# Kernel optimization log

Hardware: AMD Instinct MI355X
Metric: run time of the kernel (lower is better)

The kernel has to match this reference:

```python
import jax, jax.numpy as jnp
import numpy as np

D_MODEL = 1024
N_HEADS = 16
HEAD_DIM = D_MODEL // N_HEADS


def setup_inputs() -> dict:
    key = jax.random.key(0)
    ks = jax.random.split(key, 5)
    B, T = 4, 2048
    x = jax.random.normal(ks[0], (B, T, D_MODEL), dtype=jnp.float32)
    s = 1.0 / np.sqrt(D_MODEL)
    W_qkv = jax.random.normal(ks[1], (D_MODEL, 3 * D_MODEL), dtype=jnp.float32) * s
    b_qkv = jnp.zeros((3 * D_MODEL,), dtype=jnp.float32)
    W_out = jax.random.normal(ks[2], (D_MODEL, D_MODEL), dtype=jnp.float32) * s
    b_out = jnp.zeros((D_MODEL,), dtype=jnp.float32)
    return {"x": x, "W_qkv": W_qkv, "b_qkv": b_qkv, "W_out": W_out, "b_out": b_out}


def reference(x, W_qkv, b_qkv, W_out, b_out):
    B, T, C = x.shape
    qkv = x @ W_qkv + b_qkv                      # [B,T,3C]
    q, k, v = jnp.split(qkv, 3, axis=-1)
    # [B,T,H,Dh] -> [B,H,T,Dh]
    q = q.reshape(B, T, N_HEADS, HEAD_DIM).transpose(0, 2, 1, 3)
    k = k.reshape(B, T, N_HEADS, HEAD_DIM).transpose(0, 2, 1, 3)
    v = v.reshape(B, T, N_HEADS, HEAD_DIM).transpose(0, 2, 1, 3)
    scale = HEAD_DIM ** -0.5
    attn = jnp.einsum('bhqd,bhkd->bhqk', q, k) * scale
    causal = jnp.triu(jnp.ones((T, T), dtype=bool), k=1)
    attn = jnp.where(causal, -jnp.inf, attn)
    attn = jax.nn.softmax(attn, axis=-1)
    out = jnp.einsum('bhqk,bhkd->bhqd', attn, v)
    out = out.transpose(0, 2, 1, 3).reshape(B, T, C)
    return out @ W_out + b_out
```

## Files before the change

### kernel.cpp

```cpp
#include <hip/hip_runtime.h>
#include <hip/hip_bf16.h>


typedef unsigned short u16;
typedef unsigned int u32;
typedef __attribute__((ext_vector_type(8))) short short8;
typedef __attribute__((ext_vector_type(4))) short short4v;
typedef __attribute__((ext_vector_type(4))) float f32x4;

#define N_HEADS 16
#define HEAD_DIM 64
#define TSEQ 2048
#define BATCH 4
#define MROWS (BATCH * TSEQ)
#define N3 3072

__device__ __forceinline__ void cp16(const u16* g, u16* l) {
  __builtin_amdgcn_global_load_lds((const __attribute__((address_space(1))) void*)g,
                                   (__attribute__((address_space(3))) void*)l, 16, 0, 0);
}

__device__ __forceinline__ f32x4 mfma16(short8 a, short8 b, f32x4 c) {
  return __builtin_amdgcn_mfma_f32_16x16x32_bf16(a, b, c, 0, 0, 0);
}

__device__ __forceinline__ u16 f2b(float f) {
  __hip_bfloat16 h = __float2bfloat16(f);
  return *reinterpret_cast<u16*>(&h);
}

#define PREP_CVT_BLOCKS 8192
#define PREP_WQKV_BLOCKS (96 * 32)
#define PREP_WOUT_BLOCKS (32 * 32)
#define PREP_TOTAL (PREP_CVT_BLOCKS + PREP_WQKV_BLOCKS + PREP_WOUT_BLOCKS)

__device__ __forceinline__ void transpose_tile(const float* __restrict__ src,
                                               u16* __restrict__ dst,
                                               int R, int Cn, int c0, int r0,
                                               float (*tile)[33]) {
  const int tx = threadIdx.x & 31, ty = threadIdx.x >> 5;
  for (int i = ty; i < 32; i += 8)
    tile[i][tx] = src[(size_t)(r0 + i) * Cn + c0 + tx];
  __syncthreads();
  for (int i = ty; i < 32; i += 8)
    dst[(size_t)(c0 + i) * R + r0 + tx] = f2b(tile[tx][i]);
}

__global__ __launch_bounds__(256) void prep_kernel(
    const float* __restrict__ x, u16* __restrict__ xb,
    const float* __restrict__ Wqkv, u16* __restrict__ wqkv_t,
    const float* __restrict__ Wout, u16* __restrict__ wout_t) {
  __shared__ float tile[32][33];
  const int bx = blockIdx.x;
  if (bx < PREP_CVT_BLOCKS) {
    int i = bx * 256 + threadIdx.x;
    float4 v = *(const float4*)(x + (size_t)i * 4);
    u16* d = xb + (size_t)i * 4;
    d[0] = f2b(v.x); d[1] = f2b(v.y); d[2] = f2b(v.z); d[3] = f2b(v.w);
  } else if (bx < PREP_CVT_BLOCKS + PREP_WQKV_BLOCKS) {
    int b2 = bx - PREP_CVT_BLOCKS;
    int c0 = (b2 % 96) * 32, r0 = (b2 / 96) * 32;
    transpose_tile(Wqkv, wqkv_t, 1024, N3, c0, r0, tile);
  } else {
    int b3 = bx - PREP_CVT_BLOCKS - PREP_WQKV_BLOCKS;
    int c0 = (b3 % 32) * 32, r0 = (b3 / 32) * 32;
    transpose_tile(Wout, wout_t, 1024, 1024, c0, r0, tile);
  }
}

__device__ __forceinline__ void gemm128_sync(const u16* __restrict__ A,
                                             const u16* __restrict__ Bt,
                                             int m0, int n0,
                                             u16* Asm, u16* Bsm,
                                             f32x4 acc[4][4]) {
  const int tid = threadIdx.x;
  const int w = tid >> 6;
  const int lane = tid & 63;
  const int quad = lane >> 4;
  const int l16 = lane & 15;
  const int wm = (w >> 1) * 64;
  const int wn = (w & 1) * 64;

#pragma unroll
  for (int i = 0; i < 4; ++i)
#pragma unroll
    for (int j = 0; j < 4; ++j) acc[i][j] = (f32x4){0.f, 0.f, 0.f, 0.f};

  for (int k0 = 0; k0 < 1024; k0 += 32) {
    __syncthreads();
#pragma unroll
    for (int p = 0; p < 2; ++p) {
      int s = p * 256 + tid;
      int row = s >> 2;
      int c4 = (s & 3) ^ ((row >> 1) & 3);
      cp16(A + (size_t)(m0 + row) * 1024 + k0 + c4 * 8,
           Asm + (size_t)(p * 256 + w * 64) * 8);
      cp16(Bt + (size_t)(n0 + row) * 1024 + k0 + c4 * 8,
           Bsm + (size_t)(p * 256 + w * 64) * 8);
    }
    __syncthreads();

    short8 a[4], b[4];
#pragma unroll
    for (int i = 0; i < 4; ++i) {
      int row = wm + i * 16 + l16;
      int c4 = quad ^ ((row >> 1) & 3);
      a[i] = *(const short8*)(Asm + row * 32 + c4 * 8);
    }
#pragma unroll
    for (int j = 0; j < 4; ++j) {
      int row = wn + j * 16 + l16;
      int c4 = quad ^ ((row >> 1) & 3);
      b[j] = *(const short8*)(Bsm + row * 32 + c4 * 8);
    }
#pragma unroll
    for (int i = 0; i < 4; ++i)
#pragma unroll
      for (int j = 0; j < 4; ++j)
        acc[i][j] = mfma16(a[i], b[j], acc[i][j]);
  }
}

__device__ __forceinline__ void gemm128_pipe(const u16* __restrict__ A,
                                             const u16* __restrict__ Bt,
                                             int m0, int n0,
                                             u16* Asm, u16* Bsm,
                                             f32x4 acc[4][4]) {
  const int tid = threadIdx.x;
  const int w = tid >> 6;
  const int lane = tid & 63;
  const int quad = lane >> 4;
  const int l16 = lane & 15;
  const int wm = (w >> 1) * 64;
  const int wn = (w & 1) * 64;

#pragma unroll
  for (int i = 0; i < 4; ++i)
#pragma unroll
    for (int j = 0; j < 4; ++j) acc[i][j] = (f32x4){0.f, 0.f, 0.f, 0.f};

#define STG128(k0_, b_)                                                     \
  do {                                                                      \
    _Pragma("unroll")                                                       \
    for (int p = 0; p < 2; ++p) {                                           \
      int s = p * 256 + tid;                                                \
      int row = s >> 2;                                                     \
      int c4 = (s & 3) ^ ((row >> 1) & 3);                                  \
      cp16(A + (size_t)(m0 + row) * 1024 + (k0_) + c4 * 8,                  \
           Asm + (size_t)(b_) * 4096 + (p * 256 + w * 64) * 8);             \
      cp16(Bt + (size_t)(n0 + row) * 1024 + (k0_) + c4 * 8,                 \
           Bsm + (size_t)(b_) * 4096 + (p * 256 + w * 64) * 8);             \
    }                                                                       \
  } while (0)

  STG128(0, 0);
  STG128(32, 1);
  asm volatile("s_waitcnt vmcnt(4)" ::: "memory");
  asm volatile("s_barrier" ::: "memory");

  for (int kt = 0; kt < 32; ++kt) {
    const u16* Ab = Asm + (kt & 1) * 4096;
    const u16* Bb = Bsm + (kt & 1) * 4096;
    short8 a[4], b[4];
#pragma unroll
    for (int i = 0; i < 4; ++i) {
      int row = wm + i * 16 + l16;
      int c4 = quad ^ ((row >> 1) & 3);
      a[i] = *(const short8*)(Ab + row * 32 + c4 * 8);
    }
#pragma unroll
    for (int j = 0; j < 4; ++j) {
      int row = wn + j * 16 + l16;
      int c4 = quad ^ ((row >> 1) & 3);
      b[j] = *(const short8*)(Bb + row * 32 + c4 * 8);
    }
#pragma unroll
    for (int i = 0; i < 4; ++i)
#pragma unroll
      for (int j = 0; j < 4; ++j)
        acc[i][j] = mfma16(a[i], b[j], acc[i][j]);

    asm volatile("s_barrier" ::: "memory");
    if (kt + 2 < 32) {
      STG128((kt + 2) * 32, kt & 1);
      asm volatile("s_waitcnt vmcnt(4)" ::: "memory");
    } else if (kt + 1 < 32) {
      asm volatile("s_waitcnt vmcnt(0)" ::: "memory");
    }
    asm volatile("s_barrier" ::: "memory");
  }
#undef STG128
}

__global__ __launch_bounds__(256) void gemm_qkv_kernel(
    const u16* __restrict__ x, const u16* __restrict__ Wt,
    const float* __restrict__ bias,
    u16* __restrict__ qb, u16* __restrict__ kb, u16* __restrict__ vtb) {
  __shared__ __align__(16) u16 Asm[128 * 32];
  __shared__ __align__(16) u16 Bsm[128 * 32];
  f32x4 acc[4][4];
  const int m0 = blockIdx.y * 128;
  const int n0 = blockIdx.x * 128;
  gemm128_sync(x, Wt, m0, n0, Asm, Bsm, acc);

  const int tid = threadIdx.x;
  const int w = tid >> 6, lane = tid & 63, quad = lane >> 4, l16 = lane & 15;
  const int wm = (w >> 1) * 64, wn = (w & 1) * 64;
#pragma unroll
  for (int j = 0; j < 4; ++j) {
    int col = n0 + wn + j * 16 + l16;
    float bv = bias[col];
    int which = col >> 10;
    int rem = col & 1023;
    int h = rem >> 6, d = rem & 63;
#pragma unroll
    for (int i = 0; i < 4; ++i) {
      int m4 = m0 + wm + i * 16 + quad * 4;
      int b_ = m4 >> 11, t4 = m4 & 2047;
      int bh = b_ * N_HEADS + h;
      if (which == 2) {
        short4v pk;
#pragma unroll
        for (int r = 0; r < 4; ++r) pk[r] = (short)f2b(acc[i][j][r] + bv);
        *(short4v*)(vtb + ((size_t)((bh << 6) + d)) * TSEQ + t4) = pk;
      } else {
        u16* dst = (which == 0) ? qb : kb;
#pragma unroll
        for (int r = 0; r < 4; ++r)
          dst[((size_t)(bh * TSEQ + t4 + r) << 6) + d] = f2b(acc[i][j][r] + bv);
      }
    }
  }
}

__global__ __launch_bounds__(512, 4) void attn_kernel(const u16* __restrict__ qb,
                                                      const u16* __restrict__ kb,
                                                      const u16* __restrict__ vtb,
                                                      u16* __restrict__ ob) {
  const int flat = blockIdx.y * 8 + blockIdx.x;
  const int swz = (flat & 7) * 64 + (flat >> 3);
  const int bh = swz >> 3;
  const int p  = swz & 7;
  const int qtH = 15 - p, qtL = p;
  __shared__ __align__(16) u16 Ksm[2][4096];
  __shared__ __align__(16) u16 Vsm[2][4096];
  const int tid = threadIdx.x;
  const int w = tid >> 6, lane = tid & 63, quad = lane >> 4, l16 = lane & 15;
  const int qminH = qtH * 128 + w * 16;
  const int qminL = qtL * 128 + w * 16;

  short8 qfH0, qfH1, qfL0, qfL1;
  {
    const u16* qrH = qb + ((size_t)(bh * TSEQ + qminH + l16)) * 64;
    qfH0 = *(const short8*)(qrH + quad * 8);
    qfH1 = *(const short8*)(qrH + 32 + quad * 8);
    const u16* qrL = qb + ((size_t)(bh * TSEQ + qminL + l16)) * 64;
    qfL0 = *(const short8*)(qrL + quad * 8);
    qfL1 = *(const short8*)(qrL + 32 + quad * 8);
  }

  f32x4 oH[4], oL[4];
  float lpH = 0.f, lpL = 0.f;
#pragma unroll
  for (int j = 0; j < 4; ++j) {
    oH[j] = (f32x4){0.f, 0.f, 0.f, 0.f};
    oL[j] = (f32x4){0.f, 0.f, 0.f, 0.f};
  }
  const float cexp = 0.18033688011112042f;
  const float M = 10.0f;

  const u16* kb_bh = kb + (size_t)bh * TSEQ * 64;
  const u16* vt_bh = vtb + (size_t)bh * 64 * TSEQ;
  const int nk = 2 * qtH + 2;

#define STAGE(kt_, b_)                                                        \
  do {                                                                        \
    const u16* kbase_ = kb_bh + (size_t)((kt_) * 64) * 64;                    \
    const u16* vbase_ = vt_bh + (kt_) * 64;                                   \
    int row_ = tid >> 3;                                                      \
    int c8_ = (tid & 7) ^ (row_ & 7);                                         \
    int krow_ = (row_ & 0x23) | ((row_ & 0x0C) << 1) | ((row_ & 0x10) >> 2);  \
    cp16(kbase_ + krow_ * 64 + c8_ * 8, &Ksm[b_][w * 512]);                   \
    cp16(vbase_ + (size_t)row_ * TSEQ + c8_ * 8, &Vsm[b_][w * 512]);          \
  } while (0)

#define FRAG(qmin_, qf0_, qf1_, o_, lp_)                                      \
  do {                                                                        \
    const int qlane = (qmin_) + l16;                                          \
    f32x4 s[4];                                                               \
    _Pragma("unroll")                                                         \
    for (int j = 0; j < 4; ++j) {                                             \
      int row = j * 16 + l16;                                                 \
      int ca = quad ^ (row & 7);                                              \
      int cb = (4 + quad) ^ (row & 7);                                        \
      short8 k0 = *(const short8*)(Kb + row * 64 + ca * 8);                   \
      short8 k1 = *(const short8*)(Kb + row * 64 + cb * 8);                   \
      f32x4 z = (f32x4){0.f, 0.f, 0.f, 0.f};                                  \
      z = mfma16(k0, (qf0_), z);                                              \
      z = mfma16(k1, (qf1_), z);                                              \
      s[j] = z;                                                               \
    }                                                                         \
    if (kt * 64 + 63 > (qmin_)) {                                             \
      _Pragma("unroll")                                                       \
      for (int j = 0; j < 4; ++j) {                                           \
        _Pragma("unroll")                                                     \
        for (int r = 0; r < 4; ++r) {                                         \
          int kabs = kt * 64 + ((j >> 1) << 5) + (quad << 3) + ((j & 1) << 2) + r; \
          if (kabs > qlane) s[j][r] = -1e30f;                                 \
        }                                                                     \
      }                                                                       \
    }                                                                         \
    short8 ap0, ap1;                                                          \
    _Pragma("unroll")                                                         \
    for (int j = 0; j < 4; ++j) {                                             \
      _Pragma("unroll")                                                       \
      for (int r = 0; r < 4; ++r) {                                           \
        float p_ = __builtin_amdgcn_exp2f(__builtin_fmaf(s[j][r], cexp, -M)); \
        (lp_) += p_;                                                          \
        u16 pb = f2b(p_);                                                     \
        if (j < 2) ap0[j * 4 + r] = (short)pb;                                \
        else       ap1[(j - 2) * 4 + r] = (short)pb;                          \
      }                                                                       \
    }                                                                         \
    _Pragma("unroll")                                                         \
    for (int j = 0; j < 4; ++j) {                                             \
      int row = j * 16 + l16;                                                 \
      int ca = quad ^ (row & 7);                                              \
      int cb = (4 + quad) ^ (row & 7);                                        \
      short8 v0 = *(const short8*)(Vb + row * 64 + ca * 8);                   \
      short8 v1 = *(const short8*)(Vb + row * 64 + cb * 8);                   \
      (o_)[j] = mfma16(ap0, v0, (o_)[j]);                                     \
      (o_)[j] = mfma16(ap1, v1, (o_)[j]);                                     \
    }                                                                         \
  } while (0)

  STAGE(0, 0);

  for (int kt = 0; kt < nk; ++kt) {
    asm volatile("s_barrier" ::: "memory");
    if (kt + 1 < nk) {
      STAGE(kt + 1, (kt + 1) & 1);
      asm volatile("s_waitcnt vmcnt(2)" ::: "memory");
    } else {
      asm volatile("s_waitcnt vmcnt(0)" ::: "memory");
    }
    asm volatile("s_barrier" ::: "memory");

    const u16* Kb = Ksm[kt & 1];
    const u16* Vb = Vsm[kt & 1];

    __builtin_amdgcn_s_setprio(1);
    if (kt * 64 <= qminH + 15) FRAG(qminH, qfH0, qfH1, oH, lpH);
    if (kt * 64 <= qminL + 15) FRAG(qminL, qfL0, qfL1, oL, lpL);
    __builtin_amdgcn_s_setprio(0);
  }
#undef FRAG
#undef STAGE

  const int b_ = bh >> 4, h = bh & 15;
#define EPI(qmin_, o_, lp_)                                                   \
  do {                                                                        \
    float lp = (lp_);                                                         \
    lp += __shfl_xor(lp, 16);                                                 \
    lp += __shfl_xor(lp, 32);                                                 \
    float dn[4];                                                              \
    _Pragma("unroll")                                                         \
    for (int r = 0; r < 4; ++r)                                               \
      dn[r] = __shfl(lp, (lane & 48) + quad * 4 + r);                         \
    _Pragma("unroll")                                                         \
    for (int j = 0; j < 4; ++j) {                                             \
      _Pragma("unroll")                                                       \
      for (int r = 0; r < 4; ++r) {                                           \
        int t = (qmin_) + quad * 4 + r;                                       \
        int d = j * 16 + l16;                                                 \
        ob[((size_t)(b_ * TSEQ + t)) * 1024 + h * 64 + d] =                   \
            f2b((o_)[j][r] / dn[r]);                                          \
      }                                                                       \
    }                                                                         \
  } while (0)
  EPI(qminH, oH, lpH);
  EPI(qminL, oL, lpL);
#undef EPI
}

__global__ __launch_bounds__(256) void gemm_out_kernel(
    const u16* __restrict__ attn, const u16* __restrict__ Wt,
    const float* __restrict__ bias, float* __restrict__ out) {
  __shared__ __align__(16) u16 Asm[2 * 4096];
  __shared__ __align__(16) u16 Bsm[2 * 4096];
  f32x4 acc[4][4];
  const int flat = blockIdx.y * 8 + blockIdx.x;
  const int swz = (flat & 7) * 64 + (flat >> 3);
  const int m0 = (swz >> 3) * 128;
  const int n0 = (swz & 7) * 128;
  gemm128_pipe(attn, Wt, m0, n0, Asm, Bsm, acc);

  const int tid = threadIdx.x;
  const int w = tid >> 6, lane = tid & 63, quad = lane >> 4, l16 = lane & 15;
  const int wm = (w >> 1) * 64, wn = (w & 1) * 64;
#pragma unroll
  for (int j = 0; j < 4; ++j) {
    int col = n0 + wn + j * 16 + l16;
    float bv = bias[col];
#pragma unroll
    for (int i = 0; i < 4; ++i)
#pragma unroll
      for (int r = 0; r < 4; ++r) {
        int m = m0 + wm + i * 16 + quad * 4 + r;
        out[(size_t)m * 1024 + col] = acc[i][j][r] + bv;
      }
  }
}

extern "C" void kernel_launch(void* const* d_in, const int* in_sizes, int n_in,
                              void* d_out, int out_size, void* d_ws, size_t ws_size,
                              hipStream_t stream) {
  const float* x    = (const float*)d_in[0];
  const float* Wqkv = (const float*)d_in[1];
  const float* bqkv = (const float*)d_in[2];
  const float* Wout = (const float*)d_in[3];
  const float* bout = (const float*)d_in[4];
  float* out = (float*)d_out;

  u16* ws = (u16*)d_ws;
  u16* xb     = ws;
  u16* wqkv_t = xb + (size_t)MROWS * 1024;
  u16* wout_t = wqkv_t + (size_t)N3 * 1024;
  u16* qbuf   = wout_t + (size_t)1024 * 1024;
  u16* kbuf   = qbuf + (size_t)MROWS * 1024;
  u16* vtbuf  = kbuf + (size_t)MROWS * 1024;
  u16* obuf   = vtbuf + (size_t)MROWS * 1024;
  (void)ws_size; (void)n_in; (void)in_sizes; (void)out_size;

  prep_kernel<<<PREP_TOTAL, 256, 0, stream>>>(x, xb, Wqkv, wqkv_t, Wout, wout_t);
  gemm_qkv_kernel<<<dim3(N3 / 128, MROWS / 128), 256, 0, stream>>>(xb, wqkv_t, bqkv, qbuf, kbuf, vtbuf);
  attn_kernel<<<dim3(8, BATCH * N_HEADS), 512, 0, stream>>>(qbuf, kbuf, vtbuf, obuf);
  gemm_out_kernel<<<dim3(8, 64), 256, 0, stream>>>(obuf, wout_t, bout, out);
}
```

Before: 238.1 us.

## Use smaller 64x128 synchronous tiles for output projection GEMM

Replaces the double-buffered 128x128 pipelined GEMM in the output projection with a simple synchronous loop over 64x128 tiles. The grid doubles to 1024 blocks and the swizzled block ordering is removed. The goal is better load balance and occupancy across compute units, at the cost of losing the load/compute overlap and some per-tile data reuse.

```diff
diff --git a/kernel.cpp b/kernel.cpp
--- a/kernel.cpp
+++ b/kernel.cpp
@@ -119,77 +119,6 @@
       for (int j = 0; j < 4; ++j)
         acc[i][j] = mfma16(a[i], b[j], acc[i][j]);
   }
-}
-
-__device__ __forceinline__ void gemm128_pipe(const u16* __restrict__ A,
-                                             const u16* __restrict__ Bt,
-                                             int m0, int n0,
-                                             u16* Asm, u16* Bsm,
-                                             f32x4 acc[4][4]) {
-  const int tid = threadIdx.x;
-  const int w = tid >> 6;
-  const int lane = tid & 63;
-  const int quad = lane >> 4;
-  const int l16 = lane & 15;
-  const int wm = (w >> 1) * 64;
-  const int wn = (w & 1) * 64;
-
-#pragma unroll
-  for (int i = 0; i < 4; ++i)
-#pragma unroll
-    for (int j = 0; j < 4; ++j) acc[i][j] = (f32x4){0.f, 0.f, 0.f, 0.f};
-
-#define STG128(k0_, b_)                                                     \
-  do {                                                                      \
-    _Pragma("unroll")                                                       \
-    for (int p = 0; p < 2; ++p) {                                           \
-      int s = p * 256 + tid;                                                \
-      int row = s >> 2;                                                     \
-      int c4 = (s & 3) ^ ((row >> 1) & 3);                                  \
-      cp16(A + (size_t)(m0 + row) * 1024 + (k0_) + c4 * 8,                  \
-           Asm + (size_t)(b_) * 4096 + (p * 256 + w * 64) * 8);             \
-      cp16(Bt + (size_t)(n0 + row) * 1024 + (k0_) + c4 * 8,                 \
-           Bsm + (size_t)(b_) * 4096 + (p * 256 + w * 64) * 8);             \
-    }                                                                       \
-  } while (0)
-
-  STG128(0, 0);
-  STG128(32, 1);
-  asm volatile("s_waitcnt vmcnt(4)" ::: "memory");
-  asm volatile("s_barrier" ::: "memory");
-
-  for (int kt = 0; kt < 32; ++kt) {
-    const u16* Ab = Asm + (kt & 1) * 4096;
-    const u16* Bb = Bsm + (kt & 1) * 4096;
-    short8 a[4], b[4];
-#pragma unroll
-    for (int i = 0; i < 4; ++i) {
-      int row = wm + i * 16 + l16;
-      int c4 = quad ^ ((row >> 1) & 3);
-      a[i] = *(const short8*)(Ab + row * 32 + c4 * 8);
-    }
-#pragma unroll
-    for (int j = 0; j < 4; ++j) {
-      int row = wn + j * 16 + l16;
-      int c4 = quad ^ ((row >> 1) & 3);
-      b[j] = *(const short8*)(Bb + row * 32 + c4 * 8);
-    }
-#pragma unroll
-    for (int i = 0; i < 4; ++i)
-#pragma unroll
-      for (int j = 0; j < 4; ++j)
-        acc[i][j] = mfma16(a[i], b[j], acc[i][j]);
-
-    asm volatile("s_barrier" ::: "memory");
-    if (kt + 2 < 32) {
-      STG128((kt + 2) * 32, kt & 1);
-      asm volatile("s_waitcnt vmcnt(4)" ::: "memory");
-    } else if (kt + 1 < 32) {
-      asm volatile("s_waitcnt vmcnt(0)" ::: "memory");
-    }
-    asm volatile("s_barrier" ::: "memory");
-  }
-#undef STG128
 }
 
 __global__ __launch_bounds__(256) void gemm_qkv_kernel(
@@ -386,24 +315,64 @@
 __global__ __launch_bounds__(256) void gemm_out_kernel(
     const u16* __restrict__ attn, const u16* __restrict__ Wt,
     const float* __restrict__ bias, float* __restrict__ out) {
-  __shared__ __align__(16) u16 Asm[2 * 4096];
-  __shared__ __align__(16) u16 Bsm[2 * 4096];
-  f32x4 acc[4][4];
-  const int flat = blockIdx.y * 8 + blockIdx.x;
-  const int swz = (flat & 7) * 64 + (flat >> 3);
-  const int m0 = (swz >> 3) * 128;
-  const int n0 = (swz & 7) * 128;
-  gemm128_pipe(attn, Wt, m0, n0, Asm, Bsm, acc);
-
+  __shared__ __align__(16) u16 Asm[64 * 32];
+  __shared__ __align__(16) u16 Bsm[128 * 32];
   const int tid = threadIdx.x;
   const int w = tid >> 6, lane = tid & 63, quad = lane >> 4, l16 = lane & 15;
-  const int wm = (w >> 1) * 64, wn = (w & 1) * 64;
+  const int wm = (w >> 1) * 32, wn = (w & 1) * 64;
+  const int m0 = blockIdx.y * 64;
+  const int n0 = blockIdx.x * 128;
+
+  f32x4 acc[2][4];
+#pragma unroll
+  for (int i = 0; i < 2; ++i)
+#pragma unroll
+    for (int j = 0; j < 4; ++j) acc[i][j] = (f32x4){0.f, 0.f, 0.f, 0.f};
+
+  for (int k0 = 0; k0 < 1024; k0 += 32) {
+    __syncthreads();
+    {
+      int row = tid >> 2;
+      int c4 = (tid & 3) ^ ((row >> 1) & 3);
+      cp16(attn + (size_t)(m0 + row) * 1024 + k0 + c4 * 8,
+           Asm + (size_t)(w * 64) * 8);
+    }
+#pragma unroll
+    for (int p = 0; p < 2; ++p) {
+      int s = p * 256 + tid;
+      int row = s >> 2;
+      int c4 = (s & 3) ^ ((row >> 1) & 3);
+      cp16(Wt + (size_t)(n0 + row) * 1024 + k0 + c4 * 8,
+           Bsm + (size_t)(p * 256 + w * 64) * 8);
+    }
+    __syncthreads();
+
+    short8 a[2], b[4];
+#pragma unroll
+    for (int i = 0; i < 2; ++i) {
+      int row = wm + i * 16 + l16;
+      int c4 = quad ^ ((row >> 1) & 3);
+      a[i] = *(const short8*)(Asm + row * 32 + c4 * 8);
+    }
+#pragma unroll
+    for (int j = 0; j < 4; ++j) {
+      int row = wn + j * 16 + l16;
+      int c4 = quad ^ ((row >> 1) & 3);
+      b[j] = *(const short8*)(Bsm + row * 32 + c4 * 8);
+    }
+#pragma unroll
+    for (int i = 0; i < 2; ++i)
+#pragma unroll
+      for (int j = 0; j < 4; ++j)
+        acc[i][j] = mfma16(a[i], b[j], acc[i][j]);
+  }
+
 #pragma unroll
   for (int j = 0; j < 4; ++j) {
     int col = n0 + wn + j * 16 + l16;
     float bv = bias[col];
 #pragma unroll
-    for (int i = 0; i < 4; ++i)
+    for (int i = 0; i < 2; ++i)
 #pragma unroll
       for (int r = 0; r < 4; ++r) {
         int m = m0 + wm + i * 16 + quad * 4 + r;
@@ -435,5 +404,5 @@
   prep_kernel<<<PREP_TOTAL, 256, 0, stream>>>(x, xb, Wqkv, wqkv_t, Wout, wout_t);
   gemm_qkv_kernel<<<dim3(N3 / 128, MROWS / 128), 256, 0, stream>>>(xb, wqkv_t, bqkv, qbuf, kbuf, vtbuf);
   attn_kernel<<<dim3(8, BATCH * N_HEADS), 512, 0, stream>>>(qbuf, kbuf, vtbuf, obuf);
-  gemm_out_kernel<<<dim3(8, 64), 256, 0, stream>>>(obuf, wout_t, bout, out);
-}
+  gemm_out_kernel<<<dim3(8, 128), 256, 0, stream>>>(obuf, wout_t, bout, out);
+}
```

New measurement: 245.3 us. 1.03x slower.
